# Optimization experiments

Hardware: AMD Instinct MI355X
Metric: run time of the kernel (lower is better)

Reference implementation:

```python
import jax, jax.numpy as jnp
import numpy as np

B, N, M = 256, 2207, 16          # graphs per batch, nodes per graph, mid_channel
E = 16777216                      # total edges in the batched graph
C1, C2 = 12, 4                    # global_conv1_dim, global_conv2_dim
H1, H2 = 256, 64                  # FC hidden sizes
EPS = 1e-5                        # LayerNorm / BatchNorm eps
BN_SCALE = 1.0 / np.sqrt(1.0 + EPS)  # eval BatchNorm with running_mean=0, running_var=1


def setup_inputs() -> dict:
    ks = jax.random.split(jax.random.key(0), 16)
    def nrm(i, shape, s):
        return jax.random.normal(ks[i], shape, jnp.float32) * s
    return {
        "x": jax.random.normal(ks[0], (B * N, 1), jnp.float32),
        "edge_index": jax.random.randint(ks[1], (2, E), 0, B * N, dtype=jnp.int32),
        "edge_weight": jax.random.uniform(ks[2], (E,), jnp.float32),
        # GraphConv: lin_rel (with bias) on aggregated neighbors + lin_root on self
        "w_root": nrm(3, (1, M), 0.5),
        "w_rel": nrm(4, (1, M), 0.5),
        "b_rel": jnp.full((M,), 0.01, jnp.float32),
        # LayerNorm over (num_nodes, mid_channel)
        "ln_g": jnp.ones((N, M), jnp.float32),
        "ln_b": jnp.zeros((N, M), jnp.float32),
        # 1x1 conv stacks
        "gc1_w": nrm(5, (C1, M), 0.3), "gc1_b": nrm(6, (C1,), 0.1),
        "bn1_g": jnp.ones((C1,), jnp.float32), "bn1_b": jnp.zeros((C1,), jnp.float32),
        "gc2_w": nrm(7, (C2, C1), 0.3), "gc2_b": nrm(8, (C2,), 0.1),
        "bn2_g": jnp.ones((C2,), jnp.float32), "bn2_b": jnp.zeros((C2,), jnp.float32),
        # FC stack (weights stored [in, out])
        "fc_w1": nrm(9, (C2 * N, H1), 0.02), "fc_b1": jnp.full((H1,), 0.01, jnp.float32),
        "fbn1_g": jnp.ones((H1,), jnp.float32), "fbn1_b": jnp.zeros((H1,), jnp.float32),
        "fc_w2": nrm(10, (H1, H2), 0.1), "fc_b2": jnp.full((H2,), 0.01, jnp.float32),
        "fbn2_g": jnp.ones((H2,), jnp.float32), "fbn2_b": jnp.zeros((H2,), jnp.float32),
        "fc1_w": nrm(11, (H2, 1), 0.1), "fc1_b": jnp.full((1,), 0.01, jnp.float32),
    }


def reference(x, edge_index, edge_weight, w_root, w_rel, b_rel, ln_g, ln_b,
              gc1_w, gc1_b, bn1_g, bn1_b, gc2_w, gc2_b, bn2_g, bn2_b,
              fc_w1, fc_b1, fbn1_g, fbn1_b, fc_w2, fc_b2, fbn2_g, fbn2_b,
              fc1_w, fc1_b):
    src, dst = edge_index[0], edge_index[1]
    # GraphConv: gather source features, weight, scatter-add to destinations
    agg = jax.ops.segment_sum(x[src] * edge_weight[:, None], dst, num_segments=B * N)
    h = jax.nn.relu(agg @ w_rel + b_rel + x @ w_root)          # [B*N, M]
    h = h.reshape(B, N, M)
    # LayerNorm over (N, M) per sample (biased variance, as in torch)
    mu = h.mean(axis=(1, 2), keepdims=True)
    var = ((h - mu) ** 2).mean(axis=(1, 2), keepdims=True)
    h = (h - mu) * jax.lax.rsqrt(var + EPS) * ln_g + ln_b
    h = h.transpose(0, 2, 1)                                   # [B, M, N]
    # 1x1 conv -> relu -> eval-BN (rm=0, rv=1)
    y = jax.nn.relu(jnp.einsum('oc,bcn->bon', gc1_w, h) + gc1_b[None, :, None])
    y = y * (BN_SCALE * bn1_g)[None, :, None] + bn1_b[None, :, None]
    y = jax.nn.relu(jnp.einsum('oc,bcn->bon', gc2_w, y) + gc2_b[None, :, None])
    y = y * (BN_SCALE * bn2_g)[None, :, None] + bn2_b[None, :, None]
    z = y.reshape(B, C2 * N)                                   # channel-major flatten, matches torch view
    z = z @ fc_w1 + fc_b1
    z = jax.nn.relu(z * (BN_SCALE * fbn1_g) + fbn1_b)
    z = z @ fc_w2 + fc_b2
    z = jax.nn.relu(z * (BN_SCALE * fbn2_g) + fbn2_b)
    return z @ fc1_w + fc1_b                                   # [B, 1]
```

## Files before the change

### kernel.cpp

```cpp
#include <hip/hip_runtime.h>
#include <hip/hip_bf16.h>

#define BB   256
#define NN   2207
#define MM   16
#define EE   16777216
#define CC1  12
#define CC2  4
#define HH1  256
#define HH2  64
#define KK1  (CC2*NN)
#define LN_EPS 1e-5f
#define BN_SCALE 0.9999950000374997f
#define NBK  256
#define CAP  68096
#define MAGIC 1946067ull
#define EPB  8192
#define TPB  512

static __device__ __forceinline__ unsigned bucket_of(int d) {
    return (unsigned)(((unsigned long long)(unsigned)d * MAGIC) >> 32);
}

__global__ __launch_bounds__(TPB)
void k_bin2(const int* __restrict__ src, const int* __restrict__ dst,
            const float* __restrict__ ew, const float* __restrict__ x,
            uint2* __restrict__ pairs, unsigned int* __restrict__ glen)
{
    __shared__ uint2         pl[EPB];
    __shared__ unsigned char bl[EPB];
    __shared__ unsigned int  hist[NBK], start[NBK], cur[NBK], baseg[NBK];
    __shared__ unsigned int  wtot[4];

    const int t = threadIdx.x;
    if (t < NBK) hist[t] = 0;
    __syncthreads();

    const int i4base = blockIdx.x * (EPB/4);
    int4 dreg[4];
    #pragma unroll
    for (int q = 0; q < 4; ++q) {
        dreg[q] = reinterpret_cast<const int4*>(dst)[i4base + q*TPB + t];
        atomicAdd(&hist[bucket_of(dreg[q].x)], 1u);
        atomicAdd(&hist[bucket_of(dreg[q].y)], 1u);
        atomicAdd(&hist[bucket_of(dreg[q].z)], 1u);
        atomicAdd(&hist[bucket_of(dreg[q].w)], 1u);
    }
    __syncthreads();

    if (t < NBK) {
        unsigned h = hist[t], v = h;
        #pragma unroll
        for (int off = 1; off < 64; off <<= 1) {
            unsigned u = __shfl_up(v, off);
            if ((t & 63) >= off) v += u;
        }
        start[t] = v - h;
        if ((t & 63) == 63) wtot[t >> 6] = v;
    }
    __syncthreads();
    if (t < NBK) {
        const int w = t >> 6;
        unsigned wo = 0;
        if (w > 0) wo += wtot[0];
        if (w > 1) wo += wtot[1];
        if (w > 2) wo += wtot[2];
        start[t] += wo;
        cur[t] = 0;
        int j = (t + (blockIdx.x << 2)) & (NBK - 1);
        baseg[j] = atomicAdd(&glen[j], hist[j]);
    }
    __syncthreads();

    #define PLACE(S,D,W) { \
        unsigned b_ = bucket_of(D); \
        float v_ = x[S] * (W); \
        unsigned p_ = start[b_] + atomicAdd(&cur[b_], 1u); \
        pl[p_] = make_uint2((unsigned)((D) - (int)(b_*NN)), __float_as_uint(v_)); \
        bl[p_] = (unsigned char)b_; }
    #pragma unroll
    for (int q = 0; q < 4; ++q) {
        int i4 = i4base + q*TPB + t;
        int4   s4 = reinterpret_cast<const int4*>(src)[i4];
        float4 w4 = reinterpret_cast<const float4*>(ew)[i4];
        int4   d4 = dreg[q];
        PLACE(s4.x, d4.x, w4.x);
        PLACE(s4.y, d4.y, w4.y);
        PLACE(s4.z, d4.z, w4.z);
        PLACE(s4.w, d4.w, w4.w);
    }
    #undef PLACE
    __syncthreads();

    #pragma unroll
    for (int q = 0; q < EPB/TPB; ++q) {
        int i = q*TPB + t;
        unsigned j = bl[i];
        unsigned g = baseg[j] + ((unsigned)i - start[j]);
        if (g < CAP) pairs[(size_t)j*CAP + g] = pl[i];
    }
}

__global__ __launch_bounds__(512)
void k_sample_fused(const float* __restrict__ x,
              const uint2* __restrict__ pairs, const unsigned int* __restrict__ glen,
              const float* __restrict__ w_root, const float* __restrict__ w_rel,
              const float* __restrict__ b_rel,
              const float* __restrict__ ln_g, const float* __restrict__ ln_b,
              const float* __restrict__ gc1_w, const float* __restrict__ gc1_b,
              const float* __restrict__ bn1_g, const float* __restrict__ bn1_b,
              const float* __restrict__ gc2_w, const float* __restrict__ gc2_b,
              const float* __restrict__ bn2_g, const float* __restrict__ bn2_b,
              float* __restrict__ z)
{
    __shared__ float xs[NN], acc[NN];
    __shared__ float gw1[CC1*MM], gb1[CC1], sb1[CC1], tb1[CC1];
    __shared__ float gw2[CC2*CC1], gb2[CC2], sb2[CC2], tb2[CC2];
    __shared__ float redS[8], redQ[8];
    __shared__ float s_mu, s_rs;

    const int b = blockIdx.x, t = threadIdx.x;
    const float* xb = x + b*NN;
    for (int n = t; n < NN; n += 512) { xs[n] = xb[n]; acc[n] = 0.f; }
    if (t < CC1*MM) gw1[t] = gc1_w[t];
    if (t >= 192 && t < 192+CC1) { int o = t-192; gb1[o]=gc1_b[o]; sb1[o]=BN_SCALE*bn1_g[o]; tb1[o]=bn1_b[o]; }
    if (t >= 208 && t < 208+CC2*CC1) gw2[t-208] = gc2_w[t-208];
    if (t >= 240 && t < 240+CC2) { int p=t-240; gb2[p]=gc2_b[p]; sb2[p]=BN_SCALE*bn2_g[p]; tb2[p]=bn2_b[p]; }

    float wr[MM], br[MM], wo[MM];
    #pragma unroll
    for (int m = 0; m < MM; ++m) { wr[m]=w_rel[m]; br[m]=b_rel[m]; wo[m]=w_root[m]; }
    __syncthreads();

    const unsigned len = min(glen[b], (unsigned)CAP);
    const uint2* pp = pairs + (size_t)b*CAP;
    for (unsigned e = t; e < len; e += 512) {
        uint2 pr = pp[e];
        atomicAdd(&acc[pr.x], __uint_as_float(pr.y));
    }
    __syncthreads();

    float S = 0.f, Q = 0.f;
    for (int n = t; n < NN; n += 512) {
        float a = acc[n], xv = xs[n];
        #pragma unroll
        for (int m = 0; m < MM; ++m) {
            float h = fmaxf(fmaf(a, wr[m], fmaf(xv, wo[m], br[m])), 0.f);
            S += h; Q += h*h;
        }
    }
    #pragma unroll
    for (int off = 32; off; off >>= 1) { S += __shfl_down(S, off); Q += __shfl_down(Q, off); }
    if ((t & 63) == 0) { redS[t>>6] = S; redQ[t>>6] = Q; }
    __syncthreads();
    if (t == 0) {
        float SS = 0.f, QQ = 0.f;
        #pragma unroll
        for (int i = 0; i < 8; ++i) { SS += redS[i]; QQ += redQ[i]; }
        const float inv = 1.f / (float)(NN*MM);
        float mu = SS * inv;
        float var = QQ * inv - mu*mu;
        s_mu = mu; s_rs = rsqrtf(var + LN_EPS);
    }
    __syncthreads();
    const float mu = s_mu, rs = s_rs;

    float* zb = z + (size_t)b * KK1;
    for (int n = t; n < NN; n += 512) {
        float a = acc[n], xv = xs[n];
        float hn[MM];
        const float4* g4  = reinterpret_cast<const float4*>(ln_g + n*MM);
        const float4* be4 = reinterpret_cast<const float4*>(ln_b + n*MM);
        #pragma unroll
        for (int q = 0; q < 4; ++q) {
            float4 g = g4[q], be = be4[q];
            float gg[4]  = {g.x, g.y, g.z, g.w};
            float bb_[4] = {be.x, be.y, be.z, be.w};
            #pragma unroll
            for (int j = 0; j < 4; ++j) {
                int m = q*4 + j;
                float h = fmaxf(fmaf(a, wr[m], fmaf(xv, wo[m], br[m])), 0.f);
                hn[m] = (h - mu) * rs * gg[j] + bb_[j];
            }
        }
        float y1[CC1];
        #pragma unroll
        for (int o = 0; o < CC1; ++o) {
            float a1 = gb1[o];
            #pragma unroll
            for (int m = 0; m < MM; ++m) a1 = fmaf(gw1[o*MM+m], hn[m], a1);
            y1[o] = fmaxf(a1, 0.f) * sb1[o] + tb1[o];
        }
        #pragma unroll
        for (int p = 0; p < CC2; ++p) {
            float a2 = gb2[p];
            #pragma unroll
            for (int o = 0; o < CC1; ++o) a2 = fmaf(gw2[p*CC1+o], y1[o], a2);
            zb[p*NN + n] = fmaxf(a2, 0.f) * sb2[p] + tb2[p];
        }
    }
}

#define GK_CHUNK 288
__global__ __launch_bounds__(256)
void k_fc1_part(const float* __restrict__ z, const float* __restrict__ W1,
                float* __restrict__ out1_part)
{
    __shared__ float zs[64*36];
    __shared__ float ws_[32*68];
    const int bt = blockIdx.x, jt = blockIdx.y, ks = blockIdx.z;
    const int t = threadIdx.x;
    const int tb = t >> 4, tj = t & 15;
    const int k0 = ks * GK_CHUNK;
    const int kend = min(k0 + GK_CHUNK, KK1);
    float acc[4][4] = {};
    const int zrow = t >> 2, zcol = (t & 3) * 8;
    const int wrow = t >> 3, wcol = (t & 7) * 8;

    for (int kc = k0; kc < kend; kc += 32) {
        const float* zsrc = z + (size_t)(bt*64 + zrow)*KK1 + kc + zcol;
        #pragma unroll
        for (int q = 0; q < 2; ++q) {
            int k = kc + zcol + q*4;
            float4 v;
            if (k + 3 < kend) v = *reinterpret_cast<const float4*>(zsrc + q*4);
            else {
                v.x = (k+0 < kend) ? zsrc[q*4+0] : 0.f;
                v.y = (k+1 < kend) ? zsrc[q*4+1] : 0.f;
                v.z = (k+2 < kend) ? zsrc[q*4+2] : 0.f;
                v.w = (k+3 < kend) ? zsrc[q*4+3] : 0.f;
            }
            *reinterpret_cast<float4*>(&zs[zrow*36 + zcol + q*4]) = v;
        }
        {
            int k = kc + wrow;
            const float* wsrc = W1 + (size_t)k*HH1 + jt*64 + wcol;
            #pragma unroll
            for (int q = 0; q < 2; ++q) {
                float4 v;
                if (k < kend) v = *reinterpret_cast<const float4*>(wsrc + q*4);
                else v = float4{0.f,0.f,0.f,0.f};
                *reinterpret_cast<float4*>(&ws_[wrow*68 + wcol + q*4]) = v;
            }
        }
        __syncthreads();
        #pragma unroll
        for (int kk = 0; kk < 32; ++kk) {
            float4 w4 = *reinterpret_cast<const float4*>(&ws_[kk*68 + tj*4]);
            float zv[4], wv[4] = {w4.x, w4.y, w4.z, w4.w};
            #pragma unroll
            for (int ib = 0; ib < 4; ++ib) zv[ib] = zs[(tb*4+ib)*36 + kk];
            #pragma unroll
            for (int ib = 0; ib < 4; ++ib)
                #pragma unroll
                for (int ij = 0; ij < 4; ++ij)
                    acc[ib][ij] = fmaf(zv[ib], wv[ij], acc[ib][ij]);
        }
        __syncthreads();
    }
    #pragma unroll
    for (int ib = 0; ib < 4; ++ib) {
        int row = bt*64 + tb*4 + ib;
        float4 v = make_float4(acc[ib][0], acc[ib][1], acc[ib][2], acc[ib][3]);
        *reinterpret_cast<float4*>(
            &out1_part[((size_t)ks*256 + row)*HH1 + jt*64 + tj*4]) = v;
    }
}

__global__ __launch_bounds__(256)
void k_tail_part(const float* __restrict__ out1_part,
            const float* __restrict__ fc_b1, const float* __restrict__ fbn1_g,
            const float* __restrict__ fbn1_b,
            const float* __restrict__ W2, const float* __restrict__ fc_b2,
            const float* __restrict__ fbn2_g, const float* __restrict__ fbn2_b,
            const float* __restrict__ fc1_w, const float* __restrict__ fc1_b,
            float* __restrict__ out)
{
    __shared__ float o1s[HH1];
    const int b = blockIdx.x, t = threadIdx.x;
    float raw = fc_b1[t];
    #pragma unroll 4
    for (int ks = 0; ks < 31; ++ks)
        raw += out1_part[((size_t)ks*256 + b)*HH1 + t];
    o1s[t] = fmaxf(raw * (BN_SCALE * fbn1_g[t]) + fbn1_b[t], 0.f);
    __syncthreads();
    if (t < HH2) {
        float acc = fc_b2[t];
        #pragma unroll 4
        for (int j = 0; j < HH1; ++j) acc = fmaf(o1s[j], W2[j*HH2 + t], acc);
        float v2 = fmaxf(acc * (BN_SCALE * fbn2_g[t]) + fbn2_b[t], 0.f);
        float c = v2 * fc1_w[t];
        #pragma unroll
        for (int off = 32; off; off >>= 1) c += __shfl_down(c, off);
        if (t == 0) out[b] = c + fc1_b[0];
    }
}

__global__ __launch_bounds__(256)
void k_edge(const int* __restrict__ src, const int* __restrict__ dst,
            const float* __restrict__ ew, const float* __restrict__ x,
            float* __restrict__ agg)
{
    int i = blockIdx.x * 256 + threadIdx.x;
    const int4   s4 = reinterpret_cast<const int4*>(src)[i];
    const int4   d4 = reinterpret_cast<const int4*>(dst)[i];
    const float4 w4 = reinterpret_cast<const float4*>(ew)[i];
    unsafeAtomicAdd(&agg[d4.x], x[s4.x] * w4.x);
    unsafeAtomicAdd(&agg[d4.y], x[s4.y] * w4.y);
    unsafeAtomicAdd(&agg[d4.z], x[s4.z] * w4.z);
    unsafeAtomicAdd(&agg[d4.w], x[s4.w] * w4.w);
}

__global__ __launch_bounds__(256)
void k_sample(const float* __restrict__ x, const float* __restrict__ agg,
              const float* __restrict__ w_root, const float* __restrict__ w_rel,
              const float* __restrict__ b_rel,
              const float* __restrict__ ln_g, const float* __restrict__ ln_b,
              const float* __restrict__ gc1_w, const float* __restrict__ gc1_b,
              const float* __restrict__ bn1_g, const float* __restrict__ bn1_b,
              const float* __restrict__ gc2_w, const float* __restrict__ gc2_b,
              const float* __restrict__ bn2_g, const float* __restrict__ bn2_b,
              float* __restrict__ z)
{
    __shared__ float xs[NN], as[NN];
    __shared__ float gw1[CC1*MM], gb1[CC1], sb1[CC1], tb1[CC1];
    __shared__ float gw2[CC2*CC1], gb2[CC2], sb2[CC2], tb2[CC2];
    __shared__ float redS[4], redQ[4];
    __shared__ float s_mu, s_rs;

    const int b = blockIdx.x, t = threadIdx.x;
    const float* xb = x + b*NN;
    const float* ab = agg + b*NN;
    for (int n = t; n < NN; n += 256) { xs[n] = xb[n]; as[n] = ab[n]; }
    if (t < CC1*MM) gw1[t] = gc1_w[t];
    if (t >= 192 && t < 192+CC1) { int o = t-192; gb1[o]=gc1_b[o]; sb1[o]=BN_SCALE*bn1_g[o]; tb1[o]=bn1_b[o]; }
    if (t >= 208 && t < 208+CC2*CC1) gw2[t-208] = gc2_w[t-208];
    if (t >= 240 && t < 240+CC2) { int p=t-240; gb2[p]=gc2_b[p]; sb2[p]=BN_SCALE*bn2_g[p]; tb2[p]=bn2_b[p]; }

    float wr[MM], br[MM], wo[MM];
    #pragma unroll
    for (int m = 0; m < MM; ++m) { wr[m]=w_rel[m]; br[m]=b_rel[m]; wo[m]=w_root[m]; }
    __syncthreads();

    float S = 0.f, Q = 0.f;
    for (int n = t; n < NN; n += 256) {
        float a = as[n], xv = xs[n];
        #pragma unroll
        for (int m = 0; m < MM; ++m) {
            float h = fmaxf(fmaf(a, wr[m], fmaf(xv, wo[m], br[m])), 0.f);
            S += h; Q += h*h;
        }
    }
    #pragma unroll
    for (int off = 32; off; off >>= 1) { S += __shfl_down(S, off); Q += __shfl_down(Q, off); }
    if ((t & 63) == 0) { redS[t>>6] = S; redQ[t>>6] = Q; }
    __syncthreads();
    if (t == 0) {
        float SS = redS[0]+redS[1]+redS[2]+redS[3];
        float QQ = redQ[0]+redQ[1]+redQ[2]+redQ[3];
        const float inv = 1.f / (float)(NN*MM);
        float mu = SS * inv;
        float var = QQ * inv - mu*mu;
        s_mu = mu; s_rs = rsqrtf(var + LN_EPS);
    }
    __syncthreads();
    const float mu = s_mu, rs = s_rs;

    float* zb = z + (size_t)b * KK1;
    for (int n = t; n < NN; n += 256) {
        float a = as[n], xv = xs[n];
        float hn[MM];
        const float4* g4  = reinterpret_cast<const float4*>(ln_g + n*MM);
        const float4* be4 = reinterpret_cast<const float4*>(ln_b + n*MM);
        #pragma unroll
        for (int q = 0; q < 4; ++q) {
            float4 g = g4[q], be = be4[q];
            float gg[4]  = {g.x, g.y, g.z, g.w};
            float bb_[4] = {be.x, be.y, be.z, be.w};
            #pragma unroll
            for (int j = 0; j < 4; ++j) {
                int m = q*4 + j;
                float h = fmaxf(fmaf(a, wr[m], fmaf(xv, wo[m], br[m])), 0.f);
                hn[m] = (h - mu) * rs * gg[j] + bb_[j];
            }
        }
        float y1[CC1];
        #pragma unroll
        for (int o = 0; o < CC1; ++o) {
            float a1 = gb1[o];
            #pragma unroll
            for (int m = 0; m < MM; ++m) a1 = fmaf(gw1[o*MM+m], hn[m], a1);
            y1[o] = fmaxf(a1, 0.f) * sb1[o] + tb1[o];
        }
        #pragma unroll
        for (int p = 0; p < CC2; ++p) {
            float a2 = gb2[p];
            #pragma unroll
            for (int o = 0; o < CC1; ++o) a2 = fmaf(gw2[p*CC1+o], y1[o], a2);
            zb[p*NN + n] = fmaxf(a2, 0.f) * sb2[p] + tb2[p];
        }
    }
}

__global__ __launch_bounds__(256)
void k_fc1(const float* __restrict__ z, const float* __restrict__ W1,
           float* __restrict__ out1_raw)
{
    __shared__ float zs[64*36];
    __shared__ float ws_[32*68];
    const int bt = blockIdx.x, jt = blockIdx.y, ks = blockIdx.z;
    const int t = threadIdx.x;
    const int tb = t >> 4, tj = t & 15;
    const int k0 = ks * GK_CHUNK;
    const int kend = min(k0 + GK_CHUNK, KK1);
    float acc[4][4] = {};
    const int zrow = t >> 2, zcol = (t & 3) * 8;
    const int wrow = t >> 3, wcol = (t & 7) * 8;

    for (int kc = k0; kc < kend; kc += 32) {
        const float* zsrc = z + (size_t)(bt*64 + zrow)*KK1 + kc + zcol;
        #pragma unroll
        for (int q = 0; q < 2; ++q) {
            int k = kc + zcol + q*4;
            float4 v;
            if (k + 3 < kend) v = *reinterpret_cast<const float4*>(zsrc + q*4);
            else {
                v.x = (k+0 < kend) ? zsrc[q*4+0] : 0.f;
                v.y = (k+1 < kend) ? zsrc[q*4+1] : 0.f;
                v.z = (k+2 < kend) ? zsrc[q*4+2] : 0.f;
                v.w = (k+3 < kend) ? zsrc[q*4+3] : 0.f;
            }
            *reinterpret_cast<float4*>(&zs[zrow*36 + zcol + q*4]) = v;
        }
        {
            int k = kc + wrow;
            const float* wsrc = W1 + (size_t)k*HH1 + jt*64 + wcol;
            #pragma unroll
            for (int q = 0; q < 2; ++q) {
                float4 v;
                if (k < kend) v = *reinterpret_cast<const float4*>(wsrc + q*4);
                else v = float4{0.f,0.f,0.f,0.f};
                *reinterpret_cast<float4*>(&ws_[wrow*68 + wcol + q*4]) = v;
            }
        }
        __syncthreads();
        #pragma unroll
        for (int kk = 0; kk < 32; ++kk) {
            float4 w4 = *reinterpret_cast<const float4*>(&ws_[kk*68 + tj*4]);
            float zv[4], wv[4] = {w4.x, w4.y, w4.z, w4.w};
            #pragma unroll
            for (int ib = 0; ib < 4; ++ib) zv[ib] = zs[(tb*4+ib)*36 + kk];
            #pragma unroll
            for (int ib = 0; ib < 4; ++ib)
                #pragma unroll
                for (int ij = 0; ij < 4; ++ij)
                    acc[ib][ij] = fmaf(zv[ib], wv[ij], acc[ib][ij]);
        }
        __syncthreads();
    }
    #pragma unroll
    for (int ib = 0; ib < 4; ++ib) {
        int row = bt*64 + tb*4 + ib;
        #pragma unroll
        for (int ij = 0; ij < 4; ++ij)
            unsafeAtomicAdd(&out1_raw[row*HH1 + jt*64 + tj*4 + ij], acc[ib][ij]);
    }
}

__global__ __launch_bounds__(256)
void k_tail(const float* __restrict__ out1_raw,
            const float* __restrict__ fc_b1, const float* __restrict__ fbn1_g,
            const float* __restrict__ fbn1_b,
            const float* __restrict__ W2, const float* __restrict__ fc_b2,
            const float* __restrict__ fbn2_g, const float* __restrict__ fbn2_b,
            const float* __restrict__ fc1_w, const float* __restrict__ fc1_b,
            float* __restrict__ out)
{
    __shared__ float o1s[HH1];
    const int b = blockIdx.x, t = threadIdx.x;
    float raw = out1_raw[b*HH1 + t] + fc_b1[t];
    o1s[t] = fmaxf(raw * (BN_SCALE * fbn1_g[t]) + fbn1_b[t], 0.f);
    __syncthreads();
    if (t < HH2) {
        float acc = fc_b2[t];
        #pragma unroll 4
        for (int j = 0; j < HH1; ++j) acc = fmaf(o1s[j], W2[j*HH2 + t], acc);
        float v2 = fmaxf(acc * (BN_SCALE * fbn2_g[t]) + fbn2_b[t], 0.f);
        float c = v2 * fc1_w[t];
        #pragma unroll
        for (int off = 32; off; off >>= 1) c += __shfl_down(c, off);
        if (t == 0) out[b] = c + fc1_b[0];
    }
}

extern "C" void kernel_launch(void* const* d_in, const int* in_sizes, int n_in,
                              void* d_out, int out_size, void* d_ws, size_t ws_size,
                              hipStream_t stream)
{
    const float* x      = (const float*)d_in[0];
    const int*   ei     = (const int*)  d_in[1];
    const float* ew     = (const float*)d_in[2];
    const float* w_root = (const float*)d_in[3];
    const float* w_rel  = (const float*)d_in[4];
    const float* b_rel  = (const float*)d_in[5];
    const float* ln_g   = (const float*)d_in[6];
    const float* ln_b   = (const float*)d_in[7];
    const float* gc1_w  = (const float*)d_in[8];
    const float* gc1_b  = (const float*)d_in[9];
    const float* bn1_g  = (const float*)d_in[10];
    const float* bn1_b  = (const float*)d_in[11];
    const float* gc2_w  = (const float*)d_in[12];
    const float* gc2_b  = (const float*)d_in[13];
    const float* bn2_g  = (const float*)d_in[14];
    const float* bn2_b  = (const float*)d_in[15];
    const float* fc_w1  = (const float*)d_in[16];
    const float* fc_b1  = (const float*)d_in[17];
    const float* fbn1_g = (const float*)d_in[18];
    const float* fbn1_b = (const float*)d_in[19];
    const float* fc_w2  = (const float*)d_in[20];
    const float* fc_b2  = (const float*)d_in[21];
    const float* fbn2_g = (const float*)d_in[22];
    const float* fbn2_b = (const float*)d_in[23];
    const float* fc1_w  = (const float*)d_in[24];
    const float* fc1_b  = (const float*)d_in[25];
    float* out = (float*)d_out;

    char* ws = (char*)d_ws;
    const size_t off_pairs = 0;
    const size_t off_glen  = off_pairs + (size_t)NBK*CAP*8;
    const size_t off_zbuf  = off_glen + 4096;
    const size_t off_op    = off_zbuf + (size_t)BB*KK1*4;
    const size_t need      = off_op + (size_t)31*HH1*256*4;

    if (ws_size >= need) {
        uint2*        pairs = (uint2*)(ws + off_pairs);
        unsigned int* glen  = (unsigned int*)(ws + off_glen);
        float*        zbuf  = (float*)(ws + off_zbuf);
        float*        o1p   = (float*)(ws + off_op);

        hipMemsetAsync(glen, 0, 4096, stream);
        k_bin2<<<EE/EPB, TPB, 0, stream>>>(ei, ei + EE, ew, x, pairs, glen);
        k_sample_fused<<<BB, 512, 0, stream>>>(x, pairs, glen,
                                         w_root, w_rel, b_rel, ln_g, ln_b,
                                         gc1_w, gc1_b, bn1_g, bn1_b,
                                         gc2_w, gc2_b, bn2_g, bn2_b, zbuf);
        k_fc1_part<<<dim3(4,4,31), 256, 0, stream>>>(zbuf, fc_w1, o1p);
        k_tail_part<<<BB, 256, 0, stream>>>(o1p, fc_b1, fbn1_g, fbn1_b,
                                       fc_w2, fc_b2, fbn2_g, fbn2_b,
                                       fc1_w, fc1_b, out);
    } else {
        float* agg      = (float*)(ws);
        float* zbuf     = (float*)(ws + 2259968);
        float* out1_raw = (float*)(ws + 2259968 + 9039872);

        hipMemsetAsync(agg,      0, (size_t)BB*NN*sizeof(float),  stream);
        hipMemsetAsync(out1_raw, 0, (size_t)BB*HH1*sizeof(float), stream);

        k_edge<<<EE/4/256, 256, 0, stream>>>(ei, ei + EE, ew, x, agg);
        k_sample<<<BB, 256, 0, stream>>>(x, agg, w_root, w_rel, b_rel, ln_g, ln_b,
                                         gc1_w, gc1_b, bn1_g, bn1_b,
                                         gc2_w, gc2_b, bn2_g, bn2_b, zbuf);
        k_fc1<<<dim3(4,4,31), 256, 0, stream>>>(zbuf, fc_w1, out1_raw);
        k_tail<<<BB, 256, 0, stream>>>(out1_raw, fc_b1, fbn1_g, fbn1_b,
                                       fc_w2, fc_b2, fbn2_g, fbn2_b,
                                       fc1_w, fc1_b, out);
    }
}
```

Before: 352.4 us.

## Single-pass edge binning with register-held ranks and vectorized pair reads

The binning kernel now loads src, dst and weight once, computes the product and bucket, and records each edge's rank within its bucket from the histogram atomic. This removes the second global read pass and the separate cursor atomics. The bucket id is packed into the high bits of the local key, so the byte array is no longer needed, and it is masked off before the global write. The per-sample kernel reads pairs as uint4, handling two edges per load, with a scalar tail. The cost is more registers per thread to hold sixteen edges of state, which may lower occupancy.

```diff
diff --git a/kernel.cpp b/kernel.cpp
--- a/kernel.cpp
+++ b/kernel.cpp
@@ -17,34 +17,60 @@
 #define MAGIC 1946067ull
 #define EPB  8192
 #define TPB  512
+#define EPT  (EPB/TPB)
 
 static __device__ __forceinline__ unsigned bucket_of(int d) {
     return (unsigned)(((unsigned long long)(unsigned)d * MAGIC) >> 32);
 }
 
 __global__ __launch_bounds__(TPB)
-void k_bin2(const int* __restrict__ src, const int* __restrict__ dst,
+void k_bin3(const int* __restrict__ src, const int* __restrict__ dst,
             const float* __restrict__ ew, const float* __restrict__ x,
             uint2* __restrict__ pairs, unsigned int* __restrict__ glen)
 {
-    __shared__ uint2         pl[EPB];
-    __shared__ unsigned char bl[EPB];
-    __shared__ unsigned int  hist[NBK], start[NBK], cur[NBK], baseg[NBK];
-    __shared__ unsigned int  wtot[4];
+    __shared__ uint2        pl[EPB];
+    __shared__ unsigned int hist[NBK], start[NBK], baseg[NBK];
+    __shared__ unsigned int wtot[4];
 
     const int t = threadIdx.x;
     if (t < NBK) hist[t] = 0;
     __syncthreads();
 
     const int i4base = blockIdx.x * (EPB/4);
-    int4 dreg[4];
+
+    unsigned pk[EPT];
+    float    pv[EPT];
+    unsigned short pr[EPT];
     #pragma unroll
     for (int q = 0; q < 4; ++q) {
-        dreg[q] = reinterpret_cast<const int4*>(dst)[i4base + q*TPB + t];
-        atomicAdd(&hist[bucket_of(dreg[q].x)], 1u);
-        atomicAdd(&hist[bucket_of(dreg[q].y)], 1u);
-        atomicAdd(&hist[bucket_of(dreg[q].z)], 1u);
-        atomicAdd(&hist[bucket_of(dreg[q].w)], 1u);
+        int i4 = i4base + q*TPB + t;
+        int4   s4 = reinterpret_cast<const int4*>(src)[i4];
+        int4   d4 = reinterpret_cast<const int4*>(dst)[i4];
+        float4 w4 = reinterpret_cast<const float4*>(ew)[i4];
+        {
+            unsigned b_ = bucket_of(d4.x);
+            pk[q*4+0] = (b_ << 16) | (unsigned)(d4.x - (int)(b_*NN));
+            pv[q*4+0] = x[s4.x] * w4.x;
+            pr[q*4+0] = (unsigned short)atomicAdd(&hist[b_], 1u);
+        }
+        {
+            unsigned b_ = bucket_of(d4.y);
+            pk[q*4+1] = (b_ << 16) | (unsigned)(d4.y - (int)(b_*NN));
+            pv[q*4+1] = x[s4.y] * w4.y;
+            pr[q*4+1] = (unsigned short)atomicAdd(&hist[b_], 1u);
+        }
+        {
+            unsigned b_ = bucket_of(d4.z);
+            pk[q*4+2] = (b_ << 16) | (unsigned)(d4.z - (int)(b_*NN));
+            pv[q*4+2] = x[s4.z] * w4.z;
+            pr[q*4+2] = (unsigned short)atomicAdd(&hist[b_], 1u);
+        }
+        {
+            unsigned b_ = bucket_of(d4.w);
+            pk[q*4+3] = (b_ << 16) | (unsigned)(d4.w - (int)(b_*NN));
+            pv[q*4+3] = x[s4.w] * w4.w;
+            pr[q*4+3] = (unsigned short)atomicAdd(&hist[b_], 1u);
+        }
     }
     __syncthreads();
 
@@ -66,38 +92,25 @@
         if (w > 1) wo += wtot[1];
         if (w > 2) wo += wtot[2];
         start[t] += wo;
-        cur[t] = 0;
         int j = (t + (blockIdx.x << 2)) & (NBK - 1);
         baseg[j] = atomicAdd(&glen[j], hist[j]);
     }
     __syncthreads();
 
-    #define PLACE(S,D,W) { \
-        unsigned b_ = bucket_of(D); \
-        float v_ = x[S] * (W); \
-        unsigned p_ = start[b_] + atomicAdd(&cur[b_], 1u); \
-        pl[p_] = make_uint2((unsigned)((D) - (int)(b_*NN)), __float_as_uint(v_)); \
-        bl[p_] = (unsigned char)b_; }
-    #pragma unroll
-    for (int q = 0; q < 4; ++q) {
-        int i4 = i4base + q*TPB + t;
-        int4   s4 = reinterpret_cast<const int4*>(src)[i4];
-        float4 w4 = reinterpret_cast<const float4*>(ew)[i4];
-        int4   d4 = dreg[q];
-        PLACE(s4.x, d4.x, w4.x);
-        PLACE(s4.y, d4.y, w4.y);
-        PLACE(s4.z, d4.z, w4.z);
-        PLACE(s4.w, d4.w, w4.w);
-    }
-    #undef PLACE
-    __syncthreads();
-
-    #pragma unroll
-    for (int q = 0; q < EPB/TPB; ++q) {
+    #pragma unroll
+    for (int e = 0; e < EPT; ++e) {
+        unsigned b_ = pk[e] >> 16;
+        pl[start[b_] + (unsigned)pr[e]] = make_uint2(pk[e], __float_as_uint(pv[e]));
+    }
+    __syncthreads();
+
+    #pragma unroll
+    for (int q = 0; q < EPT; ++q) {
         int i = q*TPB + t;
-        unsigned j = bl[i];
+        uint2 r = pl[i];
+        unsigned j = r.x >> 16;
         unsigned g = baseg[j] + ((unsigned)i - start[j]);
-        if (g < CAP) pairs[(size_t)j*CAP + g] = pl[i];
+        if (g < CAP) pairs[(size_t)j*CAP + g] = make_uint2(r.x & 0xFFFFu, r.y);
     }
 }
 
@@ -134,8 +147,15 @@
 
     const unsigned len = min(glen[b], (unsigned)CAP);
     const uint2* pp = pairs + (size_t)b*CAP;
-    for (unsigned e = t; e < len; e += 512) {
-        uint2 pr = pp[e];
+    const uint4* pp4 = reinterpret_cast<const uint4*>(pp);
+    const unsigned len2 = len >> 1;
+    for (unsigned e = t; e < len2; e += 512) {
+        uint4 pr = pp4[e];
+        atomicAdd(&acc[pr.x], __uint_as_float(pr.y));
+        atomicAdd(&acc[pr.z], __uint_as_float(pr.w));
+    }
+    if (t == 0 && (len & 1u)) {
+        uint2 pr = pp[len - 1];
         atomicAdd(&acc[pr.x], __uint_as_float(pr.y));
     }
     __syncthreads();
@@ -539,7 +559,7 @@
         float*        o1p   = (float*)(ws + off_op);
 
         hipMemsetAsync(glen, 0, 4096, stream);
-        k_bin2<<<EE/EPB, TPB, 0, stream>>>(ei, ei + EE, ew, x, pairs, glen);
+        k_bin3<<<EE/EPB, TPB, 0, stream>>>(ei, ei + EE, ew, x, pairs, glen);
         k_sample_fused<<<BB, 512, 0, stream>>>(x, pairs, glen,
                                          w_root, w_rel, b_rel, ln_g, ln_b,
                                          gc1_w, gc1_b, bn1_g, bn1_b,
```

Result: no change. 356.3 us (+1.1%).
